# Optimization experiments

Measured on AMD Instinct MI355X. Metric: run time of the kernel, lower is better.

Reference implementation:

```python
import jax, jax.numpy as jnp
import numpy as np

_D, _R = 1024, 4096


def flow_multinomial(n, p):
    """n: [...], p: [..., k] -> mean [..., k], cov [..., k, k]."""
    mean = n[..., None] * p  # [..., k]
    k = p.shape[-1]
    eye = jnp.eye(k, dtype=p.dtype)
    # diag(mean) - n * p p^T
    cov = mean[..., None] * eye - n[..., None, None] * (p[..., :, None] * p[..., None, :])
    return mean, cov


def mvn_logprob(x, mean, cov):
    """Batched MVN log-prob via Cholesky. x/mean: [..., k], cov: [..., k, k]."""
    k = x.shape[-1]
    L = jnp.linalg.cholesky(cov)
    diff = (x - mean)[..., None]  # [..., k, 1]
    z = jax.lax.linalg.triangular_solve(L, diff, left_side=True, lower=True)
    quad = jnp.sum(z[..., 0] ** 2, axis=-1)
    logdet = 2.0 * jnp.sum(jnp.log(jnp.diagonal(L, axis1=-2, axis2=-1)), axis=-1)
    return -0.5 * (k * jnp.log(2.0 * jnp.pi) + logdet + quad)


def setup_inputs() -> dict:
    D, R = _D, _R
    key = jax.random.key(0)
    ks = jax.random.split(key, 20)
    u = lambda k, shape, lo, hi: jax.random.uniform(k, shape, minval=lo, maxval=hi, dtype=jnp.float32)
    N = u(ks[0], (R,), 1e6, 2e6)
    S = N * u(ks[1], (D, R), 0.4, 0.7)
    E = N * u(ks[2], (D, R), 0.005, 0.02)
    I = N * u(ks[3], (D, R), 0.005, 0.02)
    T = N * u(ks[4], (D, R), 0.002, 0.01)
    # observed flows for each transition (any finite values are valid)
    S_E = S[:-1] * u(ks[5], (D - 1, R), 0.0, 0.02)
    E_I = E[:-1] * u(ks[6], (D - 1, R), 0.1, 0.4)
    I_T = I[:-1] * u(ks[7], (D - 1, R), 0.1, 0.3)
    I_U = I[:-1] * u(ks[8], (D - 1, R), 0.1, 0.3)
    T_R = T[:-1] * u(ks[9], (D - 1, R), 0.2, 0.5)
    T_D = T[:-1] * u(ks[10], (D - 1, R), 0.0, 0.05)
    adjacency = u(ks[11], (R, R), 0.0, 1.0)
    logit_decay_E = jax.random.normal(ks[12], (), dtype=jnp.float32)
    logit_decay_I = jax.random.normal(ks[13], (), dtype=jnp.float32)
    logit_decay_T = jax.random.normal(ks[14], (), dtype=jnp.float32)
    detection_rate = u(ks[15], (D, R), 0.05, 0.95)
    recovery_rate = u(ks[16], (D, R), 0.05, 0.95)
    contagion_I = u(ks[17], (D, R), 0.1, 2.0)
    return dict(S=S, E=E, I=I, T=T, N=N, S_E=S_E, E_I=E_I, I_T=I_T, I_U=I_U,
                T_R=T_R, T_D=T_D, adjacency=adjacency,
                logit_decay_E=logit_decay_E, logit_decay_I=logit_decay_I,
                logit_decay_T=logit_decay_T, detection_rate=detection_rate,
                recovery_rate=recovery_rate, contagion_I=contagion_I)


def reference(S, E, I, T, N, S_E, E_I, I_T, I_U, T_R, T_D, adjacency,
              logit_decay_E, logit_decay_I, logit_decay_T,
              detection_rate, recovery_rate, contagion_I):
    decay_E = jax.nn.sigmoid(logit_decay_E)
    decay_I = jax.nn.sigmoid(logit_decay_I)
    decay_T = jax.nn.sigmoid(logit_decay_T)

    # states at the start of each transition t = 0 .. D-2
    So, Eo, Io, To = S[:-1], E[:-1], I[:-1], T[:-1]  # [D-1, R]

    # prob_S_E, vectorized over transitions: A @ I_t for each t
    AI = jnp.einsum('rq,tq->tr', adjacency, Io)       # [D-1, R]
    AN = adjacency @ N                                 # [R]
    p_SE = -jnp.expm1(-(contagion_I[:-1] * AI) / AN)   # [D-1, R]

    # S -> E (1-dim MVN)
    mS, cS = flow_multinomial(So, p_SE[..., None])
    lpS = mvn_logprob(S_E[..., None], mS, cS)

    # E -> I (1-dim MVN)
    p_EI = jnp.broadcast_to(decay_E, p_SE.shape)
    mE, cE = flow_multinomial(Eo, p_EI[..., None])
    lpE = mvn_logprob(E_I[..., None], mE, cE)

    # I -> (T, U) (2-dim MVN)
    det = detection_rate[:-1]
    pI = jnp.stack([det * decay_I, (1.0 - det) * decay_I], axis=-1)  # [D-1, R, 2]
    mI, cI = flow_multinomial(Io, pI)
    lpI = mvn_logprob(jnp.stack([I_T, I_U], axis=-1), mI, cI)

    # T -> (R, D) (2-dim MVN)
    rec = recovery_rate[:-1]
    pT = jnp.stack([rec * decay_T, (1.0 - rec) * decay_T], axis=-1)
    mT, cT = flow_multinomial(To, pT)
    lpT = mvn_logprob(jnp.stack([T_R, T_D], axis=-1), mT, cT)

    # sum over transitions -> per-region total log prob [R]
    return jnp.sum(lpS + lpE + lpI + lpT, axis=0)
```

## Files before the change

### kernel.cpp

```cpp
#include <hip/hip_runtime.h>
#include <hip/hip_bf16.h>
#include <math.h>

typedef __attribute__((ext_vector_type(8))) short bf16x8;
typedef __attribute__((ext_vector_type(4))) float f32x4;
typedef unsigned int u32;

__device__ inline ushort f2bf(float x) {
  union { float f; unsigned u; } c; c.f = x;
  unsigned u = c.u;
  u += 0x7fffu + ((u >> 16) & 1u);
  return (ushort)(u >> 16);
}

__device__ __forceinline__ void gl_lds16(const ushort* g, ushort* l) {
  __builtin_amdgcn_global_load_lds(
      (const __attribute__((address_space(1))) u32*)g,
      (__attribute__((address_space(3))) u32*)l, 16, 0, 0);
}

__global__ __launch_bounds__(256) void conv_I_kernel(const float* __restrict__ in,
                                                     ushort* __restrict__ out, int n) {
  int i = (blockIdx.x * 256 + threadIdx.x) * 4;
  if (i + 3 < n) {
    float4 v = *(const float4*)(in + i);
    ushort4 o;
    o.x = f2bf(v.x); o.y = f2bf(v.y); o.z = f2bf(v.z); o.w = f2bf(v.w);
    *(ushort4*)(out + i) = o;
  }
}

__global__ __launch_bounds__(256) void conv_adj_an(const float* __restrict__ adj,
                                                   const float* __restrict__ Nv,
                                                   ushort* __restrict__ adjbf,
                                                   float* __restrict__ AN, int R) {
  const int r = blockIdx.x;
  const int tid = threadIdx.x;
  const float* row = adj + (size_t)r * R;
  ushort* orow = adjbf + (size_t)r * R;
  float acc = 0.f;
  for (int q0 = tid * 4; q0 < R; q0 += 256 * 4) {
    float4 v = *(const float4*)(row + q0);
    float4 nv = *(const float4*)(Nv + q0);
    acc += v.x * nv.x + v.y * nv.y + v.z * nv.z + v.w * nv.w;
    ushort4 o;
    o.x = f2bf(v.x); o.y = f2bf(v.y); o.z = f2bf(v.z); o.w = f2bf(v.w);
    *(ushort4*)(orow + q0) = o;
  }
  #pragma unroll
  for (int off = 32; off > 0; off >>= 1) acc += __shfl_down(acc, off, 64);
  __shared__ float red[4];
  if ((tid & 63) == 0) red[tid >> 6] = acc;
  __syncthreads();
  if (tid == 0) AN[r] = red[0] + red[1] + red[2] + red[3];
}

__global__ __launch_bounds__(256) void gemm_bt_lds(const ushort* __restrict__ A,
                                                   const ushort* __restrict__ B,
                                                   float* __restrict__ C,
                                                   int M, int N, int K, int Khalf) {
  __shared__ __align__(16) ushort sA[128 * 32];
  __shared__ __align__(16) ushort sB[128 * 32];
  const int tid = threadIdx.x;
  const int bn = blockIdx.x, bm = blockIdx.y, bz = blockIdx.z;
  const int wave = tid >> 6, lane = tid & 63;
  const int wm = (wave >> 1) * 64, wn = (wave & 1) * 64;

  const int p0 = wave * 2, p1 = wave * 2 + 1;
  const int lrow = lane >> 2;
  const int scol = (lane & 3) * 8;
  const size_t kbase = (size_t)bz * Khalf + scol;
  const ushort* Ag0 = A + (size_t)(bm * 128 + p0 * 16 + lrow) * K + kbase;
  const ushort* Ag1 = A + (size_t)(bm * 128 + p1 * 16 + lrow) * K + kbase;
  const ushort* Bg0 = B + (size_t)(bn * 128 + p0 * 16 + lrow) * K + kbase;
  const ushort* Bg1 = B + (size_t)(bn * 128 + p1 * 16 + lrow) * K + kbase;
  ushort* sA0 = sA + p0 * 16 * 32;
  ushort* sA1 = sA + p1 * 16 * 32;
  ushort* sB0 = sB + p0 * 16 * 32;
  ushort* sB1 = sB + p1 * 16 * 32;

  const int fm = lane & 15, fk = (lane >> 4) * 8;

  f32x4 acc[4][4];
  #pragma unroll
  for (int i = 0; i < 4; ++i)
    #pragma unroll
    for (int j = 0; j < 4; ++j) acc[i][j] = (f32x4){0.f, 0.f, 0.f, 0.f};

  for (int k0 = 0; k0 < Khalf; k0 += 32) {
    __syncthreads();
    gl_lds16(Ag0 + k0, sA0);
    gl_lds16(Ag1 + k0, sA1);
    gl_lds16(Bg0 + k0, sB0);
    gl_lds16(Bg1 + k0, sB1);
    __syncthreads();
    bf16x8 af[4], bfr[4];
    #pragma unroll
    for (int i = 0; i < 4; ++i)
      af[i] = *(const bf16x8*)(sA + (wm + i * 16 + fm) * 32 + fk);
    #pragma unroll
    for (int j = 0; j < 4; ++j)
      bfr[j] = *(const bf16x8*)(sB + (wn + j * 16 + fm) * 32 + fk);
    #pragma unroll
    for (int i = 0; i < 4; ++i)
      #pragma unroll
      for (int j = 0; j < 4; ++j)
        acc[i][j] = __builtin_amdgcn_mfma_f32_16x16x32_bf16(af[i], bfr[j], acc[i][j], 0, 0, 0);
  }

  float* Cz = C + (size_t)bz * M * N;
  const int cm = (lane >> 4) * 4, cn = lane & 15;
  #pragma unroll
  for (int i = 0; i < 4; ++i)
    #pragma unroll
    for (int j = 0; j < 4; ++j) {
      size_t base = (size_t)(bm * 128 + wm + i * 16 + cm) * N + (bn * 128 + wn + j * 16 + cn);
      #pragma unroll
      for (int v = 0; v < 4; ++v)
        Cz[base + (size_t)v * N] = acc[i][j][v];
    }
}

__device__ __forceinline__ float elem_ll(float Sv, float Ev, float Iv, float Tv,
                                         float sev, float eiv, float itv, float iuv,
                                         float trv, float tdv, float dev, float rev,
                                         float cov, float aiv, float an_,
                                         float dE, float omE, float dI, float omI,
                                         float dT, float omT) {
  float acc;
  {
    float p = -expm1f(-(cov * aiv) / an_);
    float m = Sv * p;
    float var = m * (1.f - p);
    float d = sev - m;
    acc = __logf(var) + d * d / var;
  }
  {
    float m = Ev * dE;
    float var = m * omE;
    float d = eiv - m;
    acc += __logf(var) + d * d / var;
  }
  {
    float p1 = dev * dI, p2 = (1.f - dev) * dI;
    float d1 = itv - Iv * p1;
    float d2 = iuv - Iv * p2;
    float den = Iv * p1 * p2 * omI;
    float quad = (d1 * d1 * p2 * (1.f - p2) + 2.f * d1 * d2 * p1 * p2 +
                  d2 * d2 * p1 * (1.f - p1)) / den;
    acc += __logf(Iv * den) + quad;
  }
  {
    float p1 = rev * dT, p2 = (1.f - rev) * dT;
    float d1 = trv - Tv * p1;
    float d2 = tdv - Tv * p2;
    float den = Tv * p1 * p2 * omT;
    float quad = (d1 * d1 * p2 * (1.f - p2) + 2.f * d1 * d2 * p1 * p2 +
                  d2 * d2 * p1 * (1.f - p1)) / den;
    acc += __logf(Tv * den) + quad;
  }
  return acc;
}

__global__ __launch_bounds__(256) void logprob_kernel(
    const float* __restrict__ S, const float* __restrict__ E,
    const float* __restrict__ I, const float* __restrict__ T,
    const float* __restrict__ S_E, const float* __restrict__ E_I,
    const float* __restrict__ I_T, const float* __restrict__ I_U,
    const float* __restrict__ T_R, const float* __restrict__ T_D,
    const float* __restrict__ detr, const float* __restrict__ recr,
    const float* __restrict__ cont, const float* __restrict__ AI0,
    const float* __restrict__ AI1, const float* __restrict__ AN,
    const float* __restrict__ pldE, const float* __restrict__ pldI,
    const float* __restrict__ pldT, float* __restrict__ out, int D1, int R) {
  const int r0 = (blockIdx.x * 256 + threadIdx.x) * 4;
  if (r0 + 3 >= R + 3 - 3 && r0 >= R) return;
  const float dE = 1.f / (1.f + expf(-pldE[0]));
  const float dI = 1.f / (1.f + expf(-pldI[0]));
  const float dT = 1.f / (1.f + expf(-pldT[0]));
  const float omE = 1.f - dE, omI = 1.f - dI, omT = 1.f - dT;
  const float L2PI = 1.8378770664093453f;
  float4 an4 = *(const float4*)(AN + r0);
  float an_[4] = {an4.x, an4.y, an4.z, an4.w};
  float acc[4] = {0.f, 0.f, 0.f, 0.f};
  const int t0 = blockIdx.y * 16;
  const int t1 = min(t0 + 16, D1);
  for (int t = t0; t < t1; ++t) {
    const size_t idx = (size_t)t * R + r0;
    float4 Sv = *(const float4*)(S + idx);
    float4 Ev = *(const float4*)(E + idx);
    float4 Iv = *(const float4*)(I + idx);
    float4 Tv = *(const float4*)(T + idx);
    float4 se = *(const float4*)(S_E + idx);
    float4 ei = *(const float4*)(E_I + idx);
    float4 it = *(const float4*)(I_T + idx);
    float4 iu = *(const float4*)(I_U + idx);
    float4 tr = *(const float4*)(T_R + idx);
    float4 td = *(const float4*)(T_D + idx);
    float4 de = *(const float4*)(detr + idx);
    float4 re = *(const float4*)(recr + idx);
    float4 co = *(const float4*)(cont + idx);
    float4 a0 = *(const float4*)(AI0 + idx);
    float4 a1 = *(const float4*)(AI1 + idx);
    float ai[4] = {a0.x + a1.x, a0.y + a1.y, a0.z + a1.z, a0.w + a1.w};
    float Sa[4] = {Sv.x, Sv.y, Sv.z, Sv.w}, Ea[4] = {Ev.x, Ev.y, Ev.z, Ev.w};
    float Ia[4] = {Iv.x, Iv.y, Iv.z, Iv.w}, Ta[4] = {Tv.x, Tv.y, Tv.z, Tv.w};
    float sea[4] = {se.x, se.y, se.z, se.w}, eia[4] = {ei.x, ei.y, ei.z, ei.w};
    float ita[4] = {it.x, it.y, it.z, it.w}, iua[4] = {iu.x, iu.y, iu.z, iu.w};
    float tra[4] = {tr.x, tr.y, tr.z, tr.w}, tda[4] = {td.x, td.y, td.z, td.w};
    float dea[4] = {de.x, de.y, de.z, de.w}, rea[4] = {re.x, re.y, re.z, re.w};
    float coa[4] = {co.x, co.y, co.z, co.w};
    #pragma unroll
    for (int v = 0; v < 4; ++v)
      acc[v] += elem_ll(Sa[v], Ea[v], Ia[v], Ta[v], sea[v], eia[v], ita[v], iua[v],
                        tra[v], tda[v], dea[v], rea[v], coa[v], ai[v], an_[v],
                        dE, omE, dI, omI, dT, omT);
  }
  const float cterm = -3.f * L2PI * (float)(t1 - t0);
  #pragma unroll
  for (int v = 0; v < 4; ++v)
    atomicAdd(&out[r0 + v], -0.5f * acc[v] + cterm);
}

extern "C" void kernel_launch(void* const* d_in, const int* in_sizes, int n_in,
                              void* d_out, int out_size, void* d_ws, size_t ws_size,
                              hipStream_t stream) {
  const float* S    = (const float*)d_in[0];
  const float* E    = (const float*)d_in[1];
  const float* I    = (const float*)d_in[2];
  const float* T    = (const float*)d_in[3];
  const float* Nv   = (const float*)d_in[4];
  const float* S_E  = (const float*)d_in[5];
  const float* E_I  = (const float*)d_in[6];
  const float* I_T  = (const float*)d_in[7];
  const float* I_U  = (const float*)d_in[8];
  const float* T_R  = (const float*)d_in[9];
  const float* T_D  = (const float*)d_in[10];
  const float* adj  = (const float*)d_in[11];
  const float* ldE  = (const float*)d_in[12];
  const float* ldI  = (const float*)d_in[13];
  const float* ldT  = (const float*)d_in[14];
  const float* detr = (const float*)d_in[15];
  const float* recr = (const float*)d_in[16];
  const float* cont = (const float*)d_in[17];
  float* out = (float*)d_out;

  const int R  = in_sizes[4];
  const int D  = in_sizes[0] / R;
  const int D1 = D - 1;

  char* ws = (char*)d_ws;
  ushort* adjbf = (ushort*)ws;
  ushort* Ibf   = (ushort*)(ws + (size_t)R * R * 2);
  float*  AIbuf = (float*)(ws + (size_t)R * R * 2 + (size_t)D * R * 2);
  float*  ANbuf = (float*)((char*)AIbuf + 2 * (size_t)D * R * 4);

  const int nI = D * R;
  hipLaunchKernelGGL(conv_I_kernel, dim3(nI / 4 / 256), dim3(256), 0, stream, I, Ibf, nI);
  hipLaunchKernelGGL(conv_adj_an, dim3(R), dim3(256), 0, stream, adj, Nv, adjbf, ANbuf, R);
  hipLaunchKernelGGL(gemm_bt_lds, dim3(R / 128, D / 128, 2), dim3(256), 0, stream,
                     Ibf, adjbf, AIbuf, D, R, R, R / 2);
  hipMemsetAsync(d_out, 0, (size_t)out_size * sizeof(float), stream);
  hipLaunchKernelGGL(logprob_kernel, dim3(R / 1024, (D1 + 15) / 16), dim3(256), 0, stream,
                     S, E, I, T, S_E, E_I, I_T, I_U, T_R, T_D, detr, recr, cont,
                     AIbuf, AIbuf + (size_t)D * R, ANbuf, ldE, ldI, ldT, out, D1, R);
}
```

Measured before the change: 385.1 us.

## Fuse conversion kernels, swizzle GEMM LDS, split-K by four, shrink logprob tiles

Merges the I and adjacency bf16 conversion kernels into one launch. Applies an XOR swizzle to the GEMM's LDS tile layout to cut bank conflicts, and raises split-K from 2 to 4 when the workspace is large enough, giving the GEMM more blocks to spread across CUs. The logprob kernel now sums NS partial AI buffers and handles 2 timesteps per block instead of 16, which adds parallelism but also more atomics and more partial-sum traffic.

```diff
diff --git a/kernel.cpp b/kernel.cpp
--- a/kernel.cpp
+++ b/kernel.cpp
@@ -19,46 +19,49 @@
       (__attribute__((address_space(3))) u32*)l, 16, 0, 0);
 }
 
-__global__ __launch_bounds__(256) void conv_I_kernel(const float* __restrict__ in,
-                                                     ushort* __restrict__ out, int n) {
-  int i = (blockIdx.x * 256 + threadIdx.x) * 4;
-  if (i + 3 < n) {
-    float4 v = *(const float4*)(in + i);
-    ushort4 o;
-    o.x = f2bf(v.x); o.y = f2bf(v.y); o.z = f2bf(v.z); o.w = f2bf(v.w);
-    *(ushort4*)(out + i) = o;
-  }
-}
-
-__global__ __launch_bounds__(256) void conv_adj_an(const float* __restrict__ adj,
-                                                   const float* __restrict__ Nv,
-                                                   ushort* __restrict__ adjbf,
-                                                   float* __restrict__ AN, int R) {
-  const int r = blockIdx.x;
+__global__ __launch_bounds__(256) void conv_fused(const float* __restrict__ adj,
+                                                  const float* __restrict__ Nv,
+                                                  const float* __restrict__ I,
+                                                  ushort* __restrict__ adjbf,
+                                                  ushort* __restrict__ Ibf,
+                                                  float* __restrict__ AN,
+                                                  int R, int nI) {
+  const int bx = blockIdx.x;
   const int tid = threadIdx.x;
-  const float* row = adj + (size_t)r * R;
-  ushort* orow = adjbf + (size_t)r * R;
-  float acc = 0.f;
-  for (int q0 = tid * 4; q0 < R; q0 += 256 * 4) {
-    float4 v = *(const float4*)(row + q0);
-    float4 nv = *(const float4*)(Nv + q0);
-    acc += v.x * nv.x + v.y * nv.y + v.z * nv.z + v.w * nv.w;
-    ushort4 o;
-    o.x = f2bf(v.x); o.y = f2bf(v.y); o.z = f2bf(v.z); o.w = f2bf(v.w);
-    *(ushort4*)(orow + q0) = o;
-  }
-  #pragma unroll
-  for (int off = 32; off > 0; off >>= 1) acc += __shfl_down(acc, off, 64);
-  __shared__ float red[4];
-  if ((tid & 63) == 0) red[tid >> 6] = acc;
-  __syncthreads();
-  if (tid == 0) AN[r] = red[0] + red[1] + red[2] + red[3];
+  if (bx < R) {
+    const int r = bx;
+    const float* row = adj + (size_t)r * R;
+    ushort* orow = adjbf + (size_t)r * R;
+    float acc = 0.f;
+    for (int q0 = tid * 4; q0 < R; q0 += 256 * 4) {
+      float4 v = *(const float4*)(row + q0);
+      float4 nv = *(const float4*)(Nv + q0);
+      acc += v.x * nv.x + v.y * nv.y + v.z * nv.z + v.w * nv.w;
+      ushort4 o;
+      o.x = f2bf(v.x); o.y = f2bf(v.y); o.z = f2bf(v.z); o.w = f2bf(v.w);
+      *(ushort4*)(orow + q0) = o;
+    }
+    #pragma unroll
+    for (int off = 32; off > 0; off >>= 1) acc += __shfl_down(acc, off, 64);
+    __shared__ float red[4];
+    if ((tid & 63) == 0) red[tid >> 6] = acc;
+    __syncthreads();
+    if (tid == 0) AN[r] = red[0] + red[1] + red[2] + red[3];
+  } else {
+    int i = ((bx - R) * 256 + tid) * 4;
+    if (i + 3 < nI) {
+      float4 v = *(const float4*)(I + i);
+      ushort4 o;
+      o.x = f2bf(v.x); o.y = f2bf(v.y); o.z = f2bf(v.z); o.w = f2bf(v.w);
+      *(ushort4*)(Ibf + i) = o;
+    }
+  }
 }
 
 __global__ __launch_bounds__(256) void gemm_bt_lds(const ushort* __restrict__ A,
                                                    const ushort* __restrict__ B,
                                                    float* __restrict__ C,
-                                                   int M, int N, int K, int Khalf) {
+                                                   int M, int N, int K, int Ksplit) {
   __shared__ __align__(16) ushort sA[128 * 32];
   __shared__ __align__(16) ushort sB[128 * 32];
   const int tid = threadIdx.x;
@@ -68,8 +71,9 @@
 
   const int p0 = wave * 2, p1 = wave * 2 + 1;
   const int lrow = lane >> 2;
-  const int scol = (lane & 3) * 8;
-  const size_t kbase = (size_t)bz * Khalf + scol;
+  const int sblk = (lane & 3) ^ (lrow & 3);
+  const int scol = sblk * 8;
+  const size_t kbase = (size_t)bz * Ksplit + scol;
   const ushort* Ag0 = A + (size_t)(bm * 128 + p0 * 16 + lrow) * K + kbase;
   const ushort* Ag1 = A + (size_t)(bm * 128 + p1 * 16 + lrow) * K + kbase;
   const ushort* Bg0 = B + (size_t)(bn * 128 + p0 * 16 + lrow) * K + kbase;
@@ -79,7 +83,9 @@
   ushort* sB0 = sB + p0 * 16 * 32;
   ushort* sB1 = sB + p1 * 16 * 32;
 
-  const int fm = lane & 15, fk = (lane >> 4) * 8;
+  const int fm = lane & 15;
+  const int fkb = lane >> 4;
+  const int pblk = (fkb ^ (fm & 3)) * 8;
 
   f32x4 acc[4][4];
   #pragma unroll
@@ -87,7 +93,7 @@
     #pragma unroll
     for (int j = 0; j < 4; ++j) acc[i][j] = (f32x4){0.f, 0.f, 0.f, 0.f};
 
-  for (int k0 = 0; k0 < Khalf; k0 += 32) {
+  for (int k0 = 0; k0 < Ksplit; k0 += 32) {
     __syncthreads();
     gl_lds16(Ag0 + k0, sA0);
     gl_lds16(Ag1 + k0, sA1);
@@ -97,10 +103,10 @@
     bf16x8 af[4], bfr[4];
     #pragma unroll
     for (int i = 0; i < 4; ++i)
-      af[i] = *(const bf16x8*)(sA + (wm + i * 16 + fm) * 32 + fk);
+      af[i] = *(const bf16x8*)(sA + (wm + i * 16 + fm) * 32 + pblk);
     #pragma unroll
     for (int j = 0; j < 4; ++j)
-      bfr[j] = *(const bf16x8*)(sB + (wn + j * 16 + fm) * 32 + fk);
+      bfr[j] = *(const bf16x8*)(sB + (wn + j * 16 + fm) * 32 + pblk);
     #pragma unroll
     for (int i = 0; i < 4; ++i)
       #pragma unroll
@@ -162,6 +168,7 @@
   return acc;
 }
 
+template <int NS>
 __global__ __launch_bounds__(256) void logprob_kernel(
     const float* __restrict__ S, const float* __restrict__ E,
     const float* __restrict__ I, const float* __restrict__ T,
@@ -169,12 +176,12 @@
     const float* __restrict__ I_T, const float* __restrict__ I_U,
     const float* __restrict__ T_R, const float* __restrict__ T_D,
     const float* __restrict__ detr, const float* __restrict__ recr,
-    const float* __restrict__ cont, const float* __restrict__ AI0,
-    const float* __restrict__ AI1, const float* __restrict__ AN,
+    const float* __restrict__ cont, const float* __restrict__ AI,
+    const float* __restrict__ AN,
     const float* __restrict__ pldE, const float* __restrict__ pldI,
     const float* __restrict__ pldT, float* __restrict__ out, int D1, int R) {
   const int r0 = (blockIdx.x * 256 + threadIdx.x) * 4;
-  if (r0 + 3 >= R + 3 - 3 && r0 >= R) return;
+  const size_t sstride = (size_t)(D1 + 1) * R;
   const float dE = 1.f / (1.f + expf(-pldE[0]));
   const float dI = 1.f / (1.f + expf(-pldI[0]));
   const float dT = 1.f / (1.f + expf(-pldT[0]));
@@ -183,8 +190,8 @@
   float4 an4 = *(const float4*)(AN + r0);
   float an_[4] = {an4.x, an4.y, an4.z, an4.w};
   float acc[4] = {0.f, 0.f, 0.f, 0.f};
-  const int t0 = blockIdx.y * 16;
-  const int t1 = min(t0 + 16, D1);
+  const int t0 = blockIdx.y * 2;
+  const int t1 = min(t0 + 2, D1);
   for (int t = t0; t < t1; ++t) {
     const size_t idx = (size_t)t * R + r0;
     float4 Sv = *(const float4*)(S + idx);
@@ -200,9 +207,12 @@
     float4 de = *(const float4*)(detr + idx);
     float4 re = *(const float4*)(recr + idx);
     float4 co = *(const float4*)(cont + idx);
-    float4 a0 = *(const float4*)(AI0 + idx);
-    float4 a1 = *(const float4*)(AI1 + idx);
-    float ai[4] = {a0.x + a1.x, a0.y + a1.y, a0.z + a1.z, a0.w + a1.w};
+    float ai[4] = {0.f, 0.f, 0.f, 0.f};
+    #pragma unroll
+    for (int s = 0; s < NS; ++s) {
+      float4 a = *(const float4*)(AI + s * sstride + idx);
+      ai[0] += a.x; ai[1] += a.y; ai[2] += a.z; ai[3] += a.w;
+    }
     float Sa[4] = {Sv.x, Sv.y, Sv.z, Sv.w}, Ea[4] = {Ev.x, Ev.y, Ev.z, Ev.w};
     float Ia[4] = {Iv.x, Iv.y, Iv.z, Iv.w}, Ta[4] = {Tv.x, Tv.y, Tv.z, Tv.w};
     float sea[4] = {se.x, se.y, se.z, se.w}, eia[4] = {ei.x, ei.y, ei.z, ei.w};
@@ -253,15 +263,25 @@
   ushort* adjbf = (ushort*)ws;
   ushort* Ibf   = (ushort*)(ws + (size_t)R * R * 2);
   float*  AIbuf = (float*)(ws + (size_t)R * R * 2 + (size_t)D * R * 2);
-  float*  ANbuf = (float*)((char*)AIbuf + 2 * (size_t)D * R * 4);
+  const size_t need4 = (size_t)R * R * 2 + (size_t)D * R * 2 +
+                       4 * (size_t)D * R * 4 + (size_t)R * 4;
+  const int NS = (ws_size >= need4) ? 4 : 2;
+  float* ANbuf = (float*)((char*)AIbuf + (size_t)NS * D * R * 4);
 
   const int nI = D * R;
-  hipLaunchKernelGGL(conv_I_kernel, dim3(nI / 4 / 256), dim3(256), 0, stream, I, Ibf, nI);
-  hipLaunchKernelGGL(conv_adj_an, dim3(R), dim3(256), 0, stream, adj, Nv, adjbf, ANbuf, R);
-  hipLaunchKernelGGL(gemm_bt_lds, dim3(R / 128, D / 128, 2), dim3(256), 0, stream,
-                     Ibf, adjbf, AIbuf, D, R, R, R / 2);
+  const int convBlocks = R + nI / (256 * 4);
+  hipLaunchKernelGGL(conv_fused, dim3(convBlocks), dim3(256), 0, stream,
+                     adj, Nv, I, adjbf, Ibf, ANbuf, R, nI);
+  hipLaunchKernelGGL(gemm_bt_lds, dim3(R / 128, D / 128, NS), dim3(256), 0, stream,
+                     Ibf, adjbf, AIbuf, D, R, R, R / NS);
   hipMemsetAsync(d_out, 0, (size_t)out_size * sizeof(float), stream);
-  hipLaunchKernelGGL(logprob_kernel, dim3(R / 1024, (D1 + 15) / 16), dim3(256), 0, stream,
-                     S, E, I, T, S_E, E_I, I_T, I_U, T_R, T_D, detr, recr, cont,
-                     AIbuf, AIbuf + (size_t)D * R, ANbuf, ldE, ldI, ldT, out, D1, R);
-}
+  if (NS == 4) {
+    hipLaunchKernelGGL(logprob_kernel<4>, dim3(R / 1024, (D1 + 1) / 2), dim3(256), 0, stream,
+                       S, E, I, T, S_E, E_I, I_T, I_U, T_R, T_D, detr, recr, cont,
+                       AIbuf, ANbuf, ldE, ldI, ldT, out, D1, R);
+  } else {
+    hipLaunchKernelGGL(logprob_kernel<2>, dim3(R / 1024, (D1 + 1) / 2), dim3(256), 0, stream,
+                       S, E, I, T, S_E, E_I, I_T, I_U, T_R, T_D, detr, recr, cont,
+                       AIbuf, ANbuf, ldE, ldI, ldT, out, D1, R);
+  }
+}
```

After: 379.8 us. About the same (-1.4%).
